# Kernel optimization log

Measured on AMD Instinct MI355X. Metric: run time of the kernel, lower is better.

## Reference

```python
import jax, jax.numpy as jnp
import numpy as np

NUM_QUANTS = 256
RES_CH = 120
SKIP_CH = 240
K = 2
NUM_BLOCKS = 16
CYCLE = 8
DILATIONS = [2 ** (i % CYCLE) for i in range(NUM_BLOCKS)]


def causal_conv1d(x, w, b, dilation=1):
    # x: [B, Cin, T], w: [Cout, Cin, K], left-pad for causality
    pad = (w.shape[-1] - 1) * dilation
    y = jax.lax.conv_general_dilated(
        x, w, window_strides=(1,), padding=[(pad, 0)],
        rhs_dilation=(dilation,), dimension_numbers=('NCH', 'OIH', 'NCH'))
    return y + b[None, :, None]


def setup_inputs() -> dict:
    key = jax.random.key(0)
    ks = jax.random.split(key, 16)
    B, T = 8, 16384
    s = 0.1
    inp = {
        'waveforms': jax.random.normal(ks[0], (B, T), jnp.float32),
        'W_in': jax.random.normal(ks[1], (RES_CH, 1, 1), jnp.float32) * s,
        'b_in': jnp.zeros((RES_CH,), jnp.float32),
        'Wf': jax.random.normal(ks[2], (NUM_BLOCKS, RES_CH, RES_CH, K), jnp.float32) * s,
        'bf': jnp.zeros((NUM_BLOCKS, RES_CH), jnp.float32),
        'Wg': jax.random.normal(ks[3], (NUM_BLOCKS, RES_CH, RES_CH, K), jnp.float32) * s,
        'bg': jnp.zeros((NUM_BLOCKS, RES_CH), jnp.float32),
        'Wres': jax.random.normal(ks[4], (NUM_BLOCKS, RES_CH, RES_CH, 1), jnp.float32) * s,
        'bres': jnp.zeros((NUM_BLOCKS, RES_CH), jnp.float32),
        'Wskip': jax.random.normal(ks[5], (NUM_BLOCKS, SKIP_CH, RES_CH, 1), jnp.float32) * s,
        'bskip': jnp.zeros((NUM_BLOCKS, SKIP_CH), jnp.float32),
        'W1': jax.random.normal(ks[6], (NUM_QUANTS, SKIP_CH, 1), jnp.float32) * s,
        'b1': jnp.zeros((NUM_QUANTS,), jnp.float32),
        'W2': jax.random.normal(ks[7], (NUM_QUANTS, NUM_QUANTS, 1), jnp.float32) * s,
        'b2': jnp.zeros((NUM_QUANTS,), jnp.float32),
    }
    return inp


def reference(waveforms, W_in, b_in, Wf, bf, Wg, bg, Wres, bres, Wskip, bskip, W1, b1, W2, b2):
    # input 1x1 conv: [B, T] -> [B, RES_CH, T]
    x = causal_conv1d(waveforms[:, None, :], W_in, b_in)
    skip_sum = jnp.zeros((x.shape[0], SKIP_CH, x.shape[2]), x.dtype)
    for i in range(NUM_BLOCKS):
        d = DILATIONS[i]
        f = jnp.tanh(causal_conv1d(x, Wf[i], bf[i], d))
        g = jax.nn.sigmoid(causal_conv1d(x, Wg[i], bg[i], d))
        z = f * g  # gated activation
        skip_sum = skip_sum + causal_conv1d(z, Wskip[i], bskip[i])
        x = x + causal_conv1d(z, Wres[i], bres[i])
    h = jax.nn.relu(skip_sum)
    h = jax.nn.relu(causal_conv1d(h, W1, b1))
    logits = causal_conv1d(h, W2, b2)  # [B, NUM_QUANTS, T]
    return logits
```

## Files before the change

kernel.cpp:

```cpp
#include <hip/hip_runtime.h>
#include <cstddef>

#define TT 16384
#define NBATCH 8
#define CH 128
#define RES 120
#define SKIPC 240
#define NQ 256
#define NT 64
#define KZ 2048

typedef __attribute__((ext_vector_type(8))) short bf8;
typedef __attribute__((ext_vector_type(4))) short s4;
typedef __attribute__((ext_vector_type(4))) float f32x4;

__device__ __forceinline__ short f2bf(float f) {
  unsigned u = __builtin_bit_cast(unsigned, f);
  u += 0x7fffu + ((u >> 16) & 1u);
  return (short)(u >> 16);
}
__device__ __forceinline__ float bf2f(short s) {
  unsigned u = ((unsigned)(unsigned short)s) << 16;
  return __builtin_bit_cast(float, u);
}

__global__ void k_pack(const float* __restrict__ Wf, const float* __restrict__ Wg,
                       const float* __restrict__ Wres, const float* __restrict__ Wskip,
                       const float* __restrict__ W1, const float* __restrict__ W2,
                       const float* __restrict__ bf, const float* __restrict__ bg,
                       const float* __restrict__ bres, const float* __restrict__ bskip,
                       short* __restrict__ Afg, short* __restrict__ Ars,
                       short* __restrict__ W1p, short* __restrict__ W2p,
                       float* __restrict__ biasp,
                       short* __restrict__ Wskp, float* __restrict__ bsum, int do2) {
  const int NAFG = 16 * 256 * 256;
  const int NARS = 16 * 384 * 128;
  const int NW = 256 * 256;
  const int NBIA = 16 * (128 * 3 + 256);
  const int NWSK = 256 * 2048;
  const int total = NAFG + NARS + 2 * NW + NBIA + NWSK + 256;
  for (int idx = blockIdx.x * blockDim.x + threadIdx.x; idx < total;
       idx += gridDim.x * blockDim.x) {
    if (idx < NAFG) {
      int i = idx >> 16, rem = idx & 65535, m = rem >> 8, k = rem & 255;
      int tap = k >> 7, ci = k & 127;
      float v = 0.f;
      if (ci < 120) {
        if (m < 120) v = Wf[((i * 120 + m) * 120 + ci) * 2 + tap];
        else if (m >= 128 && m < 248) v = Wg[((i * 120 + (m - 128)) * 120 + ci) * 2 + tap];
      }
      Afg[idx] = f2bf(v);
    } else if (idx < NAFG + NARS) {
      int j = idx - NAFG;
      int i = j / 49152, rem = j % 49152, m = rem >> 7, k = rem & 127;
      float v = 0.f;
      if (k < 120) {
        if (m < 120) v = Wres[(i * 120 + m) * 120 + k];
        else if (m >= 128 && m < 368) v = Wskip[(i * 240 + (m - 128)) * 120 + k];
      }
      Ars[j] = f2bf(v);
    } else if (idx < NAFG + NARS + NW) {
      int j = idx - NAFG - NARS, q = j >> 8, k = j & 255;
      W1p[j] = f2bf(k < 240 ? W1[q * 240 + k] : 0.f);
    } else if (idx < NAFG + NARS + 2 * NW) {
      int j = idx - NAFG - NARS - NW;
      W2p[j] = f2bf(W2[j]);
    } else if (idx < NAFG + NARS + 2 * NW + NBIA) {
      int j = idx - NAFG - NARS - 2 * NW;
      float v = 0.f;
      if (j < 2048) { int i = j >> 7, c = j & 127; if (c < 120) v = bf[i * 120 + c]; }
      else if (j < 4096) { int jj = j - 2048; int i = jj >> 7, c = jj & 127; if (c < 120) v = bg[i * 120 + c]; }
      else if (j < 6144) { int jj = j - 4096; int i = jj >> 7, c = jj & 127; if (c < 120) v = bres[i * 120 + c]; }
      else { int jj = j - 6144; int i = jj >> 8, c = jj & 255; if (c < 240) v = bskip[i * 240 + c]; }
      biasp[j] = v;
    } else if (idx < NAFG + NARS + 2 * NW + NBIA + NWSK) {
      if (do2) {
        int j = idx - NAFG - NARS - 2 * NW - NBIA;
        int m = j >> 11, k = j & 2047;
        int layer = k >> 7, ci = k & 127;
        float v = 0.f;
        if (m < 240 && ci < 120) v = Wskip[((size_t)layer * 240 + m) * 120 + ci];
        Wskp[j] = f2bf(v);
      }
    } else {
      if (do2) {
        int m = idx - (NAFG + NARS + 2 * NW + NBIA + NWSK);
        float v = 0.f;
        if (m < 240)
          for (int l = 0; l < 16; l++) v += bskip[l * 240 + m];
        bsum[m] = v;
      }
    }
  }
}

__global__ void k_input(const float* __restrict__ wave, const float* __restrict__ win,
                        const float* __restrict__ bin, short* __restrict__ x0) {
  int idx = blockIdx.x * blockDim.x + threadIdx.x;
  if (idx >= NBATCH * TT) return;
  float wv = wave[idx];
  short* row = x0 + (size_t)idx * CH;
  for (int c = 0; c < CH; c += 4) {
    s4 v;
#pragma unroll
    for (int j = 0; j < 4; j++)
      v[j] = (c + j < 120) ? f2bf(win[c + j] * wv + bin[c + j]) : (short)0;
    *(s4*)(row + c) = v;
  }
}

__global__ __launch_bounds__(256) void k_res2(
    const short* __restrict__ xin, short* __restrict__ xout,
    short* __restrict__ zg,
    const short* __restrict__ Afg, const short* __restrict__ Ars,
    const float* __restrict__ biasp, int layer, int dil, int b_off) {
  __shared__ short zT[NT][136];
  const int bl = blockIdx.y;
  const int b = b_off + bl;
  const int t0 = blockIdx.x * NT;
  const int tid = threadIdx.x;
  const int lane = tid & 63, w = tid >> 6;
  const int l15 = lane & 15, l4 = lane >> 4;
  const size_t xbase = (size_t)b * TT * CH;

  f32x4 fa[2][4], ga[2][4];
#pragma unroll
  for (int i = 0; i < 2; i++)
#pragma unroll
    for (int j = 0; j < 4; j++) { fa[i][j] = (f32x4)0.f; ga[i][j] = (f32x4)0.f; }

  const short* pBd[4];
  const short* pBc[4];
  bool vld[4];
#pragma unroll
  for (int nt = 0; nt < 4; nt++) {
    int t = t0 + nt * 16 + l15;
    int ts = t - dil;
    vld[nt] = (ts >= 0);
    pBd[nt] = xin + xbase + (size_t)(vld[nt] ? ts : 0) * CH + l4 * 8;
    pBc[nt] = xin + xbase + (size_t)t * CH + l4 * 8;
  }
  const short* pAf[2];
  const short* pAg[2];
#pragma unroll
  for (int mt = 0; mt < 2; mt++) {
    pAf[mt] = Afg + (size_t)(w * 32 + mt * 16 + l15) * 256 + l4 * 8;
    pAg[mt] = Afg + (size_t)(128 + w * 32 + mt * 16 + l15) * 256 + l4 * 8;
  }
  const bf8 zv = (bf8)(short)0;
#pragma unroll
  for (int kk = 0; kk < 8; kk++) {
    const int k = kk * 32;
    bf8 Bv[4];
#pragma unroll
    for (int nt = 0; nt < 4; nt++) {
      if (kk < 4) {
        bf8 v = *(const bf8*)(pBd[nt] + k);
        Bv[nt] = vld[nt] ? v : zv;
      } else {
        Bv[nt] = *(const bf8*)(pBc[nt] + (k - 128));
      }
    }
#pragma unroll
    for (int mt = 0; mt < 2; mt++) {
      bf8 Av = *(const bf8*)(pAf[mt] + k);
      bf8 Gv = *(const bf8*)(pAg[mt] + k);
#pragma unroll
      for (int nt = 0; nt < 4; nt++) {
        fa[mt][nt] = __builtin_amdgcn_mfma_f32_16x16x32_bf16(Av, Bv[nt], fa[mt][nt], 0, 0, 0);
        ga[mt][nt] = __builtin_amdgcn_mfma_f32_16x16x32_bf16(Gv, Bv[nt], ga[mt][nt], 0, 0, 0);
      }
    }
  }

  const float* bf_ = biasp + (size_t)layer * 128;
  const float* bg_ = biasp + 2048 + (size_t)layer * 128;
#pragma unroll
  for (int mt = 0; mt < 2; mt++) {
    int mb = w * 32 + mt * 16 + l4 * 4;
#pragma unroll
    for (int nt = 0; nt < 4; nt++) {
      s4 zp;
#pragma unroll
      for (int r = 0; r < 4; r++) {
        float f = fa[mt][nt][r] + bf_[mb + r];
        float g = ga[mt][nt][r] + bg_[mb + r];
        float th = 1.f - 2.f / (__expf(2.f * f) + 1.f);
        float sg = 1.f / (1.f + __expf(-g));
        zp[r] = f2bf(th * sg);
      }
      *(s4*)&zT[nt * 16 + l15][mb] = zp;
    }
  }
  __syncthreads();

  for (int u = tid; u < NT * 16; u += 256) {
    int t = u >> 4, c8 = u & 15;
    bf8 v = *(const bf8*)&zT[t][c8 * 8];
    *(bf8*)(zg + ((size_t)(bl * TT + t0 + t) * 16 + layer) * 128 + c8 * 8) = v;
  }

  f32x4 acc[2][4];
#pragma unroll
  for (int i = 0; i < 2; i++)
#pragma unroll
    for (int j = 0; j < 4; j++) acc[i][j] = (f32x4)0.f;
  const short* pA[2];
#pragma unroll
  for (int mt = 0; mt < 2; mt++)
    pA[mt] = Ars + (size_t)(w * 32 + mt * 16 + l15) * 128 + l4 * 8;
#pragma unroll
  for (int kk = 0; kk < 4; kk++) {
    const int k = kk * 32;
    bf8 Bv[4];
#pragma unroll
    for (int nt = 0; nt < 4; nt++) Bv[nt] = *(const bf8*)&zT[nt * 16 + l15][k + l4 * 8];
#pragma unroll
    for (int mt = 0; mt < 2; mt++) {
      bf8 Av = *(const bf8*)(pA[mt] + k);
#pragma unroll
      for (int nt = 0; nt < 4; nt++)
        acc[mt][nt] = __builtin_amdgcn_mfma_f32_16x16x32_bf16(Av, Bv[nt], acc[mt][nt], 0, 0, 0);
    }
  }

  const float* br_ = biasp + 4096 + (size_t)layer * 128;
#pragma unroll
  for (int mt = 0; mt < 2; mt++) {
    int m = w * 32 + mt * 16 + l4 * 4;
#pragma unroll
    for (int nt = 0; nt < 4; nt++) {
      int t = t0 + nt * 16 + l15;
      s4 xv = *(const s4*)(xin + xbase + (size_t)t * CH + m);
      s4 ov;
#pragma unroll
      for (int r = 0; r < 4; r++)
        ov[r] = f2bf(bf2f(xv[r]) + acc[mt][nt][r] + br_[m + r]);
      *(s4*)(xout + xbase + (size_t)t * CH + m) = ov;
    }
  }
}

__global__ __launch_bounds__(256) void k_head2(
    const short* __restrict__ zg, const short* __restrict__ Wskp,
    const float* __restrict__ bsum,
    const short* __restrict__ W1p, const float* __restrict__ b1,
    const short* __restrict__ W2p, const float* __restrict__ b2,
    float* __restrict__ out, int b_off) {
  __shared__ short hT[NT][264];
  const int bl = blockIdx.y;
  const int b = b_off + bl;
  const int t0 = blockIdx.x * NT;
  const int tid = threadIdx.x;
  const int lane = tid & 63, w = tid >> 6;
  const int l15 = lane & 15, l4 = lane >> 4;

  f32x4 acc[4][4];
#pragma unroll
  for (int i = 0; i < 4; i++)
#pragma unroll
    for (int j = 0; j < 4; j++) acc[i][j] = (f32x4)0.f;

  const short* pB[4];
#pragma unroll
  for (int nt = 0; nt < 4; nt++)
    pB[nt] = zg + (size_t)(bl * TT + t0 + nt * 16 + l15) * KZ + l4 * 8;
  const short* pA[4];
#pragma unroll
  for (int mt = 0; mt < 4; mt++)
    pA[mt] = Wskp + (size_t)(w * 64 + mt * 16 + l15) * KZ + l4 * 8;
  for (int kk = 0; kk < KZ / 32; kk++) {
    const int k = kk * 32;
    bf8 Bv[4];
#pragma unroll
    for (int nt = 0; nt < 4; nt++) Bv[nt] = *(const bf8*)(pB[nt] + k);
#pragma unroll
    for (int mt = 0; mt < 4; mt++) {
      bf8 Av = *(const bf8*)(pA[mt] + k);
#pragma unroll
      for (int nt = 0; nt < 4; nt++)
        acc[mt][nt] = __builtin_amdgcn_mfma_f32_16x16x32_bf16(Av, Bv[nt], acc[mt][nt], 0, 0, 0);
    }
  }
#pragma unroll
  for (int mt = 0; mt < 4; mt++) {
    int mb = w * 64 + mt * 16 + l4 * 4;
#pragma unroll
    for (int nt = 0; nt < 4; nt++) {
      s4 hp;
#pragma unroll
      for (int r = 0; r < 4; r++)
        hp[r] = f2bf(fmaxf(acc[mt][nt][r] + bsum[mb + r], 0.f));
      *(s4*)&hT[nt * 16 + l15][mb] = hp;
    }
  }
  __syncthreads();

#pragma unroll
  for (int i = 0; i < 4; i++)
#pragma unroll
    for (int j = 0; j < 4; j++) acc[i][j] = (f32x4)0.f;
#pragma unroll
  for (int kk = 0; kk < 8; kk++) {
    const int k = kk * 32;
    bf8 Bv[4];
#pragma unroll
    for (int nt = 0; nt < 4; nt++) Bv[nt] = *(const bf8*)&hT[nt * 16 + l15][k + l4 * 8];
#pragma unroll
    for (int mt = 0; mt < 4; mt++) {
      bf8 Av = *(const bf8*)(W1p + (size_t)(w * 64 + mt * 16 + l15) * 256 + k + l4 * 8);
#pragma unroll
      for (int nt = 0; nt < 4; nt++)
        acc[mt][nt] = __builtin_amdgcn_mfma_f32_16x16x32_bf16(Av, Bv[nt], acc[mt][nt], 0, 0, 0);
    }
  }
  __syncthreads();
#pragma unroll
  for (int mt = 0; mt < 4; mt++) {
    int mb = w * 64 + mt * 16 + l4 * 4;
#pragma unroll
    for (int nt = 0; nt < 4; nt++) {
      s4 hp;
#pragma unroll
      for (int r = 0; r < 4; r++)
        hp[r] = f2bf(fmaxf(acc[mt][nt][r] + b1[mb + r], 0.f));
      *(s4*)&hT[nt * 16 + l15][mb] = hp;
    }
  }
  __syncthreads();

#pragma unroll
  for (int i = 0; i < 4; i++)
#pragma unroll
    for (int j = 0; j < 4; j++) acc[i][j] = (f32x4)0.f;
#pragma unroll
  for (int kk = 0; kk < 8; kk++) {
    const int k = kk * 32;
    bf8 Bv[4];
#pragma unroll
    for (int nt = 0; nt < 4; nt++) Bv[nt] = *(const bf8*)&hT[nt * 16 + l15][k + l4 * 8];
#pragma unroll
    for (int mt = 0; mt < 4; mt++) {
      bf8 Av = *(const bf8*)(W2p + (size_t)(w * 64 + mt * 16 + l15) * 256 + k + l4 * 8);
#pragma unroll
      for (int nt = 0; nt < 4; nt++)
        acc[mt][nt] = __builtin_amdgcn_mfma_f32_16x16x32_bf16(Av, Bv[nt], acc[mt][nt], 0, 0, 0);
    }
  }
#pragma unroll
  for (int mt = 0; mt < 4; mt++) {
    int q = w * 64 + mt * 16 + l4 * 4;
#pragma unroll
    for (int nt = 0; nt < 4; nt++) {
      int t = t0 + nt * 16 + l15;
#pragma unroll
      for (int r = 0; r < 4; r++)
        out[((size_t)b * NQ + q + r) * TT + t] = acc[mt][nt][r] + b2[q + r];
    }
  }
}

__global__ __launch_bounds__(256) void k_res_mfma(
    const short* __restrict__ xin, short* __restrict__ xout,
    float* __restrict__ skip,
    const short* __restrict__ Afg, const short* __restrict__ Ars,
    const float* __restrict__ biasp, int layer, int dil, int first) {
  __shared__ short zT[NT][136];
  const int b = blockIdx.y;
  const int t0 = blockIdx.x * NT;
  const int tid = threadIdx.x;
  const int lane = tid & 63, w = tid >> 6;
  const int l15 = lane & 15, l4 = lane >> 4;
  const size_t xbase = (size_t)b * TT * CH;

  f32x4 fa[2][4], ga[2][4];
#pragma unroll
  for (int i = 0; i < 2; i++)
#pragma unroll
    for (int j = 0; j < 4; j++) { fa[i][j] = (f32x4)0.f; ga[i][j] = (f32x4)0.f; }

  const short* pBd[4];
  const short* pBc[4];
  bool vld[4];
#pragma unroll
  for (int nt = 0; nt < 4; nt++) {
    int t = t0 + nt * 16 + l15;
    int ts = t - dil;
    vld[nt] = (ts >= 0);
    pBd[nt] = xin + xbase + (size_t)(vld[nt] ? ts : 0) * CH + l4 * 8;
    pBc[nt] = xin + xbase + (size_t)t * CH + l4 * 8;
  }
  const short* pAf[2];
  const short* pAg[2];
#pragma unroll
  for (int mt = 0; mt < 2; mt++) {
    pAf[mt] = Afg + (size_t)(w * 32 + mt * 16 + l15) * 256 + l4 * 8;
    pAg[mt] = Afg + (size_t)(128 + w * 32 + mt * 16 + l15) * 256 + l4 * 8;
  }
  const bf8 zv = (bf8)(short)0;
#pragma unroll
  for (int kk = 0; kk < 8; kk++) {
    const int k = kk * 32;
    bf8 Bv[4];
#pragma unroll
    for (int nt = 0; nt < 4; nt++) {
      if (kk < 4) {
        bf8 v = *(const bf8*)(pBd[nt] + k);
        Bv[nt] = vld[nt] ? v : zv;
      } else {
        Bv[nt] = *(const bf8*)(pBc[nt] + (k - 128));
      }
    }
#pragma unroll
    for (int mt = 0; mt < 2; mt++) {
      bf8 Av = *(const bf8*)(pAf[mt] + k);
      bf8 Gv = *(const bf8*)(pAg[mt] + k);
#pragma unroll
      for (int nt = 0; nt < 4; nt++) {
        fa[mt][nt] = __builtin_amdgcn_mfma_f32_16x16x32_bf16(Av, Bv[nt], fa[mt][nt], 0, 0, 0);
        ga[mt][nt] = __builtin_amdgcn_mfma_f32_16x16x32_bf16(Gv, Bv[nt], ga[mt][nt], 0, 0, 0);
      }
    }
  }

  const float* bf_ = biasp + (size_t)layer * 128;
  const float* bg_ = biasp + 2048 + (size_t)layer * 128;
#pragma unroll
  for (int mt = 0; mt < 2; mt++) {
    int mb = w * 32 + mt * 16 + l4 * 4;
#pragma unroll
    for (int nt = 0; nt < 4; nt++) {
      s4 zp;
#pragma unroll
      for (int r = 0; r < 4; r++) {
        float f = fa[mt][nt][r] + bf_[mb + r];
        float g = ga[mt][nt][r] + bg_[mb + r];
        float th = 1.f - 2.f / (__expf(2.f * f) + 1.f);
        float sg = 1.f / (1.f + __expf(-g));
        zp[r] = f2bf(th * sg);
      }
      *(s4*)&zT[nt * 16 + l15][mb] = zp;
    }
  }
  __syncthreads();

  f32x4 acc[6][4];
#pragma unroll
  for (int i = 0; i < 6; i++)
#pragma unroll
    for (int j = 0; j < 4; j++) acc[i][j] = (f32x4)0.f;
  const short* pA[6];
#pragma unroll
  for (int mt = 0; mt < 6; mt++)
    pA[mt] = Ars + (size_t)(w * 96 + mt * 16 + l15) * 128 + l4 * 8;
#pragma unroll
  for (int kk = 0; kk < 4; kk++) {
    const int k = kk * 32;
    bf8 Bv[4];
#pragma unroll
    for (int nt = 0; nt < 4; nt++) Bv[nt] = *(const bf8*)&zT[nt * 16 + l15][k + l4 * 8];
#pragma unroll
    for (int mt = 0; mt < 6; mt++) {
      bf8 Av = *(const bf8*)(pA[mt] + k);
#pragma unroll
      for (int nt = 0; nt < 4; nt++)
        acc[mt][nt] = __builtin_amdgcn_mfma_f32_16x16x32_bf16(Av, Bv[nt], acc[mt][nt], 0, 0, 0);
    }
  }

  const float* br_ = biasp + 4096 + (size_t)layer * 128;
  const float* bs_ = biasp + 6144 + (size_t)layer * 256;
#pragma unroll
  for (int mt = 0; mt < 6; mt++) {
    int m = w * 96 + mt * 16 + l4 * 4;
#pragma unroll
    for (int nt = 0; nt < 4; nt++) {
      int t = t0 + nt * 16 + l15;
      if (m < 128) {
        s4 xv = *(const s4*)(xin + xbase + (size_t)t * CH + m);
        s4 ov;
#pragma unroll
        for (int r = 0; r < 4; r++)
          ov[r] = f2bf(bf2f(xv[r]) + acc[mt][nt][r] + br_[m + r]);
        *(s4*)(xout + xbase + (size_t)t * CH + m) = ov;
      } else if (m < 128 + SKIPC) {
        int c = m - 128;
        float* sp = skip + ((size_t)b * NQ + c) * TT + t;
#pragma unroll
        for (int r = 0; r < 4; r++) {
          float v = acc[mt][nt][r] + bs_[c + r];
          if (!first) v += sp[(size_t)r * TT];
          sp[(size_t)r * TT] = v;
        }
      }
    }
  }
}

__global__ __launch_bounds__(256) void k_head_mfma(
    const float* skip, const short* __restrict__ W1p, const float* __restrict__ b1,
    const short* __restrict__ W2p, const float* __restrict__ b2, float* out) {
  __shared__ short hT[NT][264];
  __shared__ short h2T[NT][264];
  const int b = blockIdx.y;
  const int t0 = blockIdx.x * NT;
  const int tid = threadIdx.x;
  const int lane = tid & 63, w = tid >> 6;
  const int l15 = lane & 15, l4 = lane >> 4;

  for (int u = tid; u < 256 * 16; u += 256) {
    int c = u >> 4, tq = u & 15;
    if (c < SKIPC) {
      f32x4 v = *(const f32x4*)(skip + ((size_t)b * NQ + c) * TT + t0 + tq * 4);
#pragma unroll
      for (int j = 0; j < 4; j++) hT[tq * 4 + j][c] = f2bf(fmaxf(v[j], 0.f));
    } else {
#pragma unroll
      for (int j = 0; j < 4; j++) hT[tq * 4 + j][c] = 0;
    }
  }
  __syncthreads();

  f32x4 acc[4][4];
#pragma unroll
  for (int i = 0; i < 4; i++)
#pragma unroll
    for (int j = 0; j < 4; j++) acc[i][j] = (f32x4)0.f;
#pragma unroll
  for (int kk = 0; kk < 8; kk++) {
    const int k = kk * 32;
    bf8 Bv[4];
#pragma unroll
    for (int nt = 0; nt < 4; nt++) Bv[nt] = *(const bf8*)&hT[nt * 16 + l15][k + l4 * 8];
#pragma unroll
    for (int mt = 0; mt < 4; mt++) {
      bf8 Av = *(const bf8*)(W1p + (size_t)(w * 64 + mt * 16 + l15) * 256 + k + l4 * 8);
#pragma unroll
      for (int nt = 0; nt < 4; nt++)
        acc[mt][nt] = __builtin_amdgcn_mfma_f32_16x16x32_bf16(Av, Bv[nt], acc[mt][nt], 0, 0, 0);
    }
  }
#pragma unroll
  for (int mt = 0; mt < 4; mt++) {
    int mb = w * 64 + mt * 16 + l4 * 4;
#pragma unroll
    for (int nt = 0; nt < 4; nt++) {
      s4 hp;
#pragma unroll
      for (int r = 0; r < 4; r++) hp[r] = f2bf(fmaxf(acc[mt][nt][r] + b1[mb + r], 0.f));
      *(s4*)&h2T[nt * 16 + l15][mb] = hp;
    }
  }
  __syncthreads();

#pragma unroll
  for (int i = 0; i < 4; i++)
#pragma unroll
    for (int j = 0; j < 4; j++) acc[i][j] = (f32x4)0.f;
#pragma unroll
  for (int kk = 0; kk < 8; kk++) {
    const int k = kk * 32;
    bf8 Bv[4];
#pragma unroll
    for (int nt = 0; nt < 4; nt++) Bv[nt] = *(const bf8*)&h2T[nt * 16 + l15][k + l4 * 8];
#pragma unroll
    for (int mt = 0; mt < 4; mt++) {
      bf8 Av = *(const bf8*)(W2p + (size_t)(w * 64 + mt * 16 + l15) * 256 + k + l4 * 8);
#pragma unroll
      for (int nt = 0; nt < 4; nt++)
        acc[mt][nt] = __builtin_amdgcn_mfma_f32_16x16x32_bf16(Av, Bv[nt], acc[mt][nt], 0, 0, 0);
    }
  }
#pragma unroll
  for (int mt = 0; mt < 4; mt++) {
    int q = w * 64 + mt * 16 + l4 * 4;
#pragma unroll
    for (int nt = 0; nt < 4; nt++) {
      int t = t0 + nt * 16 + l15;
#pragma unroll
      for (int r = 0; r < 4; r++)
        out[((size_t)b * NQ + q + r) * TT + t] = acc[mt][nt][r] + b2[q + r];
    }
  }
}

extern "C" void kernel_launch(void* const* d_in, const int* in_sizes, int n_in,
                              void* d_out, int out_size, void* d_ws, size_t ws_size,
                              hipStream_t stream) {
  const float* wave  = (const float*)d_in[0];
  const float* W_in  = (const float*)d_in[1];
  const float* b_in  = (const float*)d_in[2];
  const float* Wf    = (const float*)d_in[3];
  const float* bf    = (const float*)d_in[4];
  const float* Wg    = (const float*)d_in[5];
  const float* bg    = (const float*)d_in[6];
  const float* Wres  = (const float*)d_in[7];
  const float* bres  = (const float*)d_in[8];
  const float* Wskip = (const float*)d_in[9];
  const float* bskip = (const float*)d_in[10];
  const float* W1    = (const float*)d_in[11];
  const float* b1    = (const float*)d_in[12];
  const float* W2    = (const float*)d_in[13];
  const float* b2    = (const float*)d_in[14];
  float* out = (float*)d_out;

  char* ws = (char*)d_ws;
  short* xA    = (short*)ws;
  short* xB    = (short*)(ws + 33554432);
  short* Afg   = (short*)(ws + 67108864);
  short* Ars   = (short*)(ws + 69206016);
  short* W1p   = (short*)(ws + 70778880);
  short* W2p   = (short*)(ws + 70909952);
  float* biasp = (float*)(ws + 71041024);
  short* Wskp  = (short*)(ws + 71081984);
  float* bsum  = (float*)(ws + 72130560);
  short* zg    = (short*)(ws + 72131584);
  const size_t BASE = 72131584ull;
  const size_t ZPB  = (size_t)TT * KZ * 2;

  int nbg = 0;
  if      (ws_size >= BASE + 8 * ZPB) nbg = 8;
  else if (ws_size >= BASE + 4 * ZPB) nbg = 4;
  else if (ws_size >= BASE + 2 * ZPB) nbg = 2;
  else if (ws_size >= BASE + 1 * ZPB) nbg = 1;
  const int do2 = (ws_size >= BASE) ? 1 : 0;

  k_pack<<<1024, 256, 0, stream>>>(Wf, Wg, Wres, Wskip, W1, W2, bf, bg, bres, bskip,
                                   Afg, Ars, W1p, W2p, biasp, Wskp, bsum, do2);
  k_input<<<(NBATCH * TT) / 256, 256, 0, stream>>>(wave, W_in, b_in, xA);

  static const int dils[16] = {1, 2, 4, 8, 16, 32, 64, 128,
                               1, 2, 4, 8, 16, 32, 64, 128};
  if (nbg > 0) {
    for (int g = 0; g < NBATCH; g += nbg) {
      const short* xi = xA;
      short* xo = xB;
      for (int i = 0; i < 16; i++) {
        k_res2<<<dim3(TT / NT, nbg), 256, 0, stream>>>(
            xi, xo, zg, Afg + (size_t)i * 65536, Ars + (size_t)i * 49152,
            biasp, i, dils[i], g);
        short* tmp = (short*)xi; xi = xo; xo = tmp;
      }
      k_head2<<<dim3(TT / NT, nbg), 256, 0, stream>>>(zg, Wskp, bsum, W1p, b1,
                                                      W2p, b2, out, g);
    }
  } else {
    const short* xi = xA;
    short* xo = xB;
    for (int i = 0; i < 16; i++) {
      k_res_mfma<<<dim3(TT / NT, NBATCH), 256, 0, stream>>>(
          xi, xo, out, Afg + (size_t)i * 65536, Ars + (size_t)i * 49152,
          biasp, i, dils[i], i == 0 ? 1 : 0);
      short* tmp = (short*)xi; xi = xo; xo = tmp;
    }
    k_head_mfma<<<dim3(TT / NT, NBATCH), 256, 0, stream>>>(out, W1p, b1, W2p, b2, out);
  }
}
```

Before: 2.278 ms.

## Halve time tiles, stage inputs in LDS, double-buffer skip GEMM in head

Reduces the time tile of the residual and head kernels from 64 to 32 so twice as many blocks launch. The residual kernel now stages the current and dilated input rows in shared memory and reuses the staged current row for the residual add, instead of reloading from global memory. The head kernel double-buffers 256-wide chunks of the gated activations in shared memory rather than reading them directly from global. The zg and output stores become nontemporal. Smaller tiles reload weights more often per output, and the extra LDS use may lower occupancy.

```diff
diff --git a/kernel.cpp b/kernel.cpp
--- a/kernel.cpp
+++ b/kernel.cpp
@@ -7,7 +7,8 @@
 #define RES 120
 #define SKIPC 240
 #define NQ 256
-#define NT 64
+#define NT2 32
+#define NTF 64
 #define KZ 2048
 
 typedef __attribute__((ext_vector_type(8))) short bf8;
@@ -114,10 +115,280 @@
     short* __restrict__ zg,
     const short* __restrict__ Afg, const short* __restrict__ Ars,
     const float* __restrict__ biasp, int layer, int dil, int b_off) {
-  __shared__ short zT[NT][136];
+  __shared__ short xc[NT2][136];
+  __shared__ short xd[NT2][136];
+  __shared__ short zT[NT2][136];
   const int bl = blockIdx.y;
   const int b = b_off + bl;
-  const int t0 = blockIdx.x * NT;
+  const int t0 = blockIdx.x * NT2;
+  const int tid = threadIdx.x;
+  const int lane = tid & 63, w = tid >> 6;
+  const int l15 = lane & 15, l4 = lane >> 4;
+  const size_t xbase = (size_t)b * TT * CH;
+
+#pragma unroll
+  for (int j = 0; j < 2; j++) {
+    int i = tid + j * 256;
+    int t = i >> 4, c8 = i & 15;
+    *(bf8*)&xc[t][c8 * 8] = *(const bf8*)(xin + xbase + (size_t)(t0 + t) * CH + c8 * 8);
+    int ts = t0 + t - dil;
+    bf8 vd = (bf8)(short)0;
+    if (ts >= 0) vd = *(const bf8*)(xin + xbase + (size_t)ts * CH + c8 * 8);
+    *(bf8*)&xd[t][c8 * 8] = vd;
+  }
+  __syncthreads();
+
+  f32x4 fa[2][2], ga[2][2];
+#pragma unroll
+  for (int i = 0; i < 2; i++)
+#pragma unroll
+    for (int j = 0; j < 2; j++) { fa[i][j] = (f32x4)0.f; ga[i][j] = (f32x4)0.f; }
+  const short* pAf[2];
+  const short* pAg[2];
+#pragma unroll
+  for (int mt = 0; mt < 2; mt++) {
+    pAf[mt] = Afg + (size_t)(w * 32 + mt * 16 + l15) * 256 + l4 * 8;
+    pAg[mt] = Afg + (size_t)(128 + w * 32 + mt * 16 + l15) * 256 + l4 * 8;
+  }
+#pragma unroll
+  for (int kk = 0; kk < 8; kk++) {
+    const int k = kk * 32;
+    bf8 Bv[2];
+#pragma unroll
+    for (int nt = 0; nt < 2; nt++)
+      Bv[nt] = (kk < 4) ? *(const bf8*)&xd[nt * 16 + l15][k + l4 * 8]
+                        : *(const bf8*)&xc[nt * 16 + l15][(k - 128) + l4 * 8];
+#pragma unroll
+    for (int mt = 0; mt < 2; mt++) {
+      bf8 Av = *(const bf8*)(pAf[mt] + k);
+      bf8 Gv = *(const bf8*)(pAg[mt] + k);
+#pragma unroll
+      for (int nt = 0; nt < 2; nt++) {
+        fa[mt][nt] = __builtin_amdgcn_mfma_f32_16x16x32_bf16(Av, Bv[nt], fa[mt][nt], 0, 0, 0);
+        ga[mt][nt] = __builtin_amdgcn_mfma_f32_16x16x32_bf16(Gv, Bv[nt], ga[mt][nt], 0, 0, 0);
+      }
+    }
+  }
+
+  const float* bf_ = biasp + (size_t)layer * 128;
+  const float* bg_ = biasp + 2048 + (size_t)layer * 128;
+#pragma unroll
+  for (int mt = 0; mt < 2; mt++) {
+    const int mb = w * 32 + mt * 16 + l4 * 4;
+#pragma unroll
+    for (int nt = 0; nt < 2; nt++) {
+      s4 zp;
+#pragma unroll
+      for (int r = 0; r < 4; r++) {
+        float f = fa[mt][nt][r] + bf_[mb + r];
+        float g = ga[mt][nt][r] + bg_[mb + r];
+        float th = 1.f - 2.f / (__expf(2.f * f) + 1.f);
+        float sg = 1.f / (1.f + __expf(-g));
+        zp[r] = f2bf(th * sg);
+      }
+      *(s4*)&zT[nt * 16 + l15][mb] = zp;
+    }
+  }
+  __syncthreads();
+
+#pragma unroll
+  for (int j = 0; j < 2; j++) {
+    int i = tid + j * 256;
+    int t = i >> 4, c8 = i & 15;
+    bf8 v = *(const bf8*)&zT[t][c8 * 8];
+    __builtin_nontemporal_store(
+        v, (bf8*)(zg + ((size_t)(bl * TT + t0 + t) * 16 + layer) * 128 + c8 * 8));
+  }
+
+  f32x4 acc[2][2];
+#pragma unroll
+  for (int i = 0; i < 2; i++)
+#pragma unroll
+    for (int j = 0; j < 2; j++) acc[i][j] = (f32x4)0.f;
+  const short* pA[2];
+#pragma unroll
+  for (int mt = 0; mt < 2; mt++)
+    pA[mt] = Ars + (size_t)(w * 32 + mt * 16 + l15) * 128 + l4 * 8;
+#pragma unroll
+  for (int kk = 0; kk < 4; kk++) {
+    const int k = kk * 32;
+    bf8 Bv[2];
+#pragma unroll
+    for (int nt = 0; nt < 2; nt++) Bv[nt] = *(const bf8*)&zT[nt * 16 + l15][k + l4 * 8];
+#pragma unroll
+    for (int mt = 0; mt < 2; mt++) {
+      bf8 Av = *(const bf8*)(pA[mt] + k);
+#pragma unroll
+      for (int nt = 0; nt < 2; nt++)
+        acc[mt][nt] = __builtin_amdgcn_mfma_f32_16x16x32_bf16(Av, Bv[nt], acc[mt][nt], 0, 0, 0);
+    }
+  }
+
+  const float* br_ = biasp + 4096 + (size_t)layer * 128;
+#pragma unroll
+  for (int mt = 0; mt < 2; mt++) {
+    const int m = w * 32 + mt * 16 + l4 * 4;
+#pragma unroll
+    for (int nt = 0; nt < 2; nt++) {
+      int t = t0 + nt * 16 + l15;
+      s4 xv = *(const s4*)&xc[nt * 16 + l15][m];
+      s4 ov;
+#pragma unroll
+      for (int r = 0; r < 4; r++)
+        ov[r] = f2bf(bf2f(xv[r]) + acc[mt][nt][r] + br_[m + r]);
+      *(s4*)(xout + xbase + (size_t)t * CH + m) = ov;
+    }
+  }
+}
+
+__global__ __launch_bounds__(256) void k_head2(
+    const short* __restrict__ zg, const short* __restrict__ Wskp,
+    const float* __restrict__ bsum,
+    const short* __restrict__ W1p, const float* __restrict__ b1,
+    const short* __restrict__ W2p, const float* __restrict__ b2,
+    float* __restrict__ out, int b_off) {
+  __shared__ short bufA[NT2][264];
+  __shared__ short bufB[NT2][264];
+  const int bl = blockIdx.y;
+  const int b = b_off + bl;
+  const int t0 = blockIdx.x * NT2;
+  const int tid = threadIdx.x;
+  const int lane = tid & 63, w = tid >> 6;
+  const int l15 = lane & 15, l4 = lane >> 4;
+
+  f32x4 acc[4][2];
+#pragma unroll
+  for (int i = 0; i < 4; i++)
+#pragma unroll
+    for (int j = 0; j < 2; j++) acc[i][j] = (f32x4)0.f;
+
+  const short* zrow = zg + (size_t)(bl * TT + t0) * KZ;
+
+#pragma unroll
+  for (int j = 0; j < 4; j++) {
+    int i = tid + j * 256;
+    int t = i >> 5, c8 = i & 31;
+    *(bf8*)&bufA[t][c8 * 8] = *(const bf8*)(zrow + (size_t)t * KZ + c8 * 8);
+  }
+  __syncthreads();
+  for (int c = 0; c < 8; c++) {
+    short (*cur)[264] = (c & 1) ? bufB : bufA;
+    short (*nxt)[264] = (c & 1) ? bufA : bufB;
+    if (c < 7) {
+#pragma unroll
+      for (int j = 0; j < 4; j++) {
+        int i = tid + j * 256;
+        int t = i >> 5, c8 = i & 31;
+        *(bf8*)&nxt[t][c8 * 8] =
+            *(const bf8*)(zrow + (size_t)t * KZ + (c + 1) * 256 + c8 * 8);
+      }
+    }
+#pragma unroll
+    for (int kk = 0; kk < 8; kk++) {
+      const int k = kk * 32;
+      bf8 Bv[2];
+#pragma unroll
+      for (int nt = 0; nt < 2; nt++)
+        Bv[nt] = *(const bf8*)&cur[nt * 16 + l15][k + l4 * 8];
+#pragma unroll
+      for (int mt = 0; mt < 4; mt++) {
+        bf8 Av = *(const bf8*)(Wskp + (size_t)(w * 64 + mt * 16 + l15) * KZ +
+                               c * 256 + k + l4 * 8);
+#pragma unroll
+        for (int nt = 0; nt < 2; nt++)
+          acc[mt][nt] = __builtin_amdgcn_mfma_f32_16x16x32_bf16(Av, Bv[nt], acc[mt][nt], 0, 0, 0);
+      }
+    }
+    __syncthreads();
+  }
+
+#pragma unroll
+  for (int mt = 0; mt < 4; mt++) {
+    const int mb = w * 64 + mt * 16 + l4 * 4;
+#pragma unroll
+    for (int nt = 0; nt < 2; nt++) {
+      s4 hp;
+#pragma unroll
+      for (int r = 0; r < 4; r++)
+        hp[r] = f2bf(fmaxf(acc[mt][nt][r] + bsum[mb + r], 0.f));
+      *(s4*)&bufA[nt * 16 + l15][mb] = hp;
+    }
+  }
+  __syncthreads();
+
+#pragma unroll
+  for (int i = 0; i < 4; i++)
+#pragma unroll
+    for (int j = 0; j < 2; j++) acc[i][j] = (f32x4)0.f;
+#pragma unroll
+  for (int kk = 0; kk < 8; kk++) {
+    const int k = kk * 32;
+    bf8 Bv[2];
+#pragma unroll
+    for (int nt = 0; nt < 2; nt++) Bv[nt] = *(const bf8*)&bufA[nt * 16 + l15][k + l4 * 8];
+#pragma unroll
+    for (int mt = 0; mt < 4; mt++) {
+      bf8 Av = *(const bf8*)(W1p + (size_t)(w * 64 + mt * 16 + l15) * 256 + k + l4 * 8);
+#pragma unroll
+      for (int nt = 0; nt < 2; nt++)
+        acc[mt][nt] = __builtin_amdgcn_mfma_f32_16x16x32_bf16(Av, Bv[nt], acc[mt][nt], 0, 0, 0);
+    }
+  }
+#pragma unroll
+  for (int mt = 0; mt < 4; mt++) {
+    const int mb = w * 64 + mt * 16 + l4 * 4;
+#pragma unroll
+    for (int nt = 0; nt < 2; nt++) {
+      s4 hp;
+#pragma unroll
+      for (int r = 0; r < 4; r++)
+        hp[r] = f2bf(fmaxf(acc[mt][nt][r] + b1[mb + r], 0.f));
+      *(s4*)&bufB[nt * 16 + l15][mb] = hp;
+    }
+  }
+  __syncthreads();
+
+#pragma unroll
+  for (int i = 0; i < 4; i++)
+#pragma unroll
+    for (int j = 0; j < 2; j++) acc[i][j] = (f32x4)0.f;
+#pragma unroll
+  for (int kk = 0; kk < 8; kk++) {
+    const int k = kk * 32;
+    bf8 Bv[2];
+#pragma unroll
+    for (int nt = 0; nt < 2; nt++) Bv[nt] = *(const bf8*)&bufB[nt * 16 + l15][k + l4 * 8];
+#pragma unroll
+    for (int mt = 0; mt < 4; mt++) {
+      bf8 Av = *(const bf8*)(W2p + (size_t)(w * 64 + mt * 16 + l15) * 256 + k + l4 * 8);
+#pragma unroll
+      for (int nt = 0; nt < 2; nt++)
+        acc[mt][nt] = __builtin_amdgcn_mfma_f32_16x16x32_bf16(Av, Bv[nt], acc[mt][nt], 0, 0, 0);
+    }
+  }
+#pragma unroll
+  for (int mt = 0; mt < 4; mt++) {
+    const int q = w * 64 + mt * 16 + l4 * 4;
+#pragma unroll
+    for (int nt = 0; nt < 2; nt++) {
+      int t = t0 + nt * 16 + l15;
+#pragma unroll
+      for (int r = 0; r < 4; r++) {
+        float v = acc[mt][nt][r] + b2[q + r];
+        __builtin_nontemporal_store(v, out + ((size_t)b * NQ + q + r) * TT + t);
+      }
+    }
+  }
+}
+
+__global__ __launch_bounds__(256) void k_res_mfma(
+    const short* __restrict__ xin, short* __restrict__ xout,
+    float* __restrict__ skip,
+    const short* __restrict__ Afg, const short* __restrict__ Ars,
+    const float* __restrict__ biasp, int layer, int dil, int first) {
+  __shared__ short zT[NTF][136];
+  const int b = blockIdx.y;
+  const int t0 = blockIdx.x * NTF;
   const int tid = threadIdx.x;
   const int lane = tid & 63, w = tid >> 6;
   const int l15 = lane & 15, l4 = lane >> 4;
@@ -194,256 +465,6 @@
   }
   __syncthreads();
 
-  for (int u = tid; u < NT * 16; u += 256) {
-    int t = u >> 4, c8 = u & 15;
-    bf8 v = *(const bf8*)&zT[t][c8 * 8];
-    *(bf8*)(zg + ((size_t)(bl * TT + t0 + t) * 16 + layer) * 128 + c8 * 8) = v;
-  }
-
-  f32x4 acc[2][4];
-#pragma unroll
-  for (int i = 0; i < 2; i++)
-#pragma unroll
-    for (int j = 0; j < 4; j++) acc[i][j] = (f32x4)0.f;
-  const short* pA[2];
-#pragma unroll
-  for (int mt = 0; mt < 2; mt++)
-    pA[mt] = Ars + (size_t)(w * 32 + mt * 16 + l15) * 128 + l4 * 8;
-#pragma unroll
-  for (int kk = 0; kk < 4; kk++) {
-    const int k = kk * 32;
-    bf8 Bv[4];
-#pragma unroll
-    for (int nt = 0; nt < 4; nt++) Bv[nt] = *(const bf8*)&zT[nt * 16 + l15][k + l4 * 8];
-#pragma unroll
-    for (int mt = 0; mt < 2; mt++) {
-      bf8 Av = *(const bf8*)(pA[mt] + k);
-#pragma unroll
-      for (int nt = 0; nt < 4; nt++)
-        acc[mt][nt] = __builtin_amdgcn_mfma_f32_16x16x32_bf16(Av, Bv[nt], acc[mt][nt], 0, 0, 0);
-    }
-  }
-
-  const float* br_ = biasp + 4096 + (size_t)layer * 128;
-#pragma unroll
-  for (int mt = 0; mt < 2; mt++) {
-    int m = w * 32 + mt * 16 + l4 * 4;
-#pragma unroll
-    for (int nt = 0; nt < 4; nt++) {
-      int t = t0 + nt * 16 + l15;
-      s4 xv = *(const s4*)(xin + xbase + (size_t)t * CH + m);
-      s4 ov;
-#pragma unroll
-      for (int r = 0; r < 4; r++)
-        ov[r] = f2bf(bf2f(xv[r]) + acc[mt][nt][r] + br_[m + r]);
-      *(s4*)(xout + xbase + (size_t)t * CH + m) = ov;
-    }
-  }
-}
-
-__global__ __launch_bounds__(256) void k_head2(
-    const short* __restrict__ zg, const short* __restrict__ Wskp,
-    const float* __restrict__ bsum,
-    const short* __restrict__ W1p, const float* __restrict__ b1,
-    const short* __restrict__ W2p, const float* __restrict__ b2,
-    float* __restrict__ out, int b_off) {
-  __shared__ short hT[NT][264];
-  const int bl = blockIdx.y;
-  const int b = b_off + bl;
-  const int t0 = blockIdx.x * NT;
-  const int tid = threadIdx.x;
-  const int lane = tid & 63, w = tid >> 6;
-  const int l15 = lane & 15, l4 = lane >> 4;
-
-  f32x4 acc[4][4];
-#pragma unroll
-  for (int i = 0; i < 4; i++)
-#pragma unroll
-    for (int j = 0; j < 4; j++) acc[i][j] = (f32x4)0.f;
-
-  const short* pB[4];
-#pragma unroll
-  for (int nt = 0; nt < 4; nt++)
-    pB[nt] = zg + (size_t)(bl * TT + t0 + nt * 16 + l15) * KZ + l4 * 8;
-  const short* pA[4];
-#pragma unroll
-  for (int mt = 0; mt < 4; mt++)
-    pA[mt] = Wskp + (size_t)(w * 64 + mt * 16 + l15) * KZ + l4 * 8;
-  for (int kk = 0; kk < KZ / 32; kk++) {
-    const int k = kk * 32;
-    bf8 Bv[4];
-#pragma unroll
-    for (int nt = 0; nt < 4; nt++) Bv[nt] = *(const bf8*)(pB[nt] + k);
-#pragma unroll
-    for (int mt = 0; mt < 4; mt++) {
-      bf8 Av = *(const bf8*)(pA[mt] + k);
-#pragma unroll
-      for (int nt = 0; nt < 4; nt++)
-        acc[mt][nt] = __builtin_amdgcn_mfma_f32_16x16x32_bf16(Av, Bv[nt], acc[mt][nt], 0, 0, 0);
-    }
-  }
-#pragma unroll
-  for (int mt = 0; mt < 4; mt++) {
-    int mb = w * 64 + mt * 16 + l4 * 4;
-#pragma unroll
-    for (int nt = 0; nt < 4; nt++) {
-      s4 hp;
-#pragma unroll
-      for (int r = 0; r < 4; r++)
-        hp[r] = f2bf(fmaxf(acc[mt][nt][r] + bsum[mb + r], 0.f));
-      *(s4*)&hT[nt * 16 + l15][mb] = hp;
-    }
-  }
-  __syncthreads();
-
-#pragma unroll
-  for (int i = 0; i < 4; i++)
-#pragma unroll
-    for (int j = 0; j < 4; j++) acc[i][j] = (f32x4)0.f;
-#pragma unroll
-  for (int kk = 0; kk < 8; kk++) {
-    const int k = kk * 32;
-    bf8 Bv[4];
-#pragma unroll
-    for (int nt = 0; nt < 4; nt++) Bv[nt] = *(const bf8*)&hT[nt * 16 + l15][k + l4 * 8];
-#pragma unroll
-    for (int mt = 0; mt < 4; mt++) {
-      bf8 Av = *(const bf8*)(W1p + (size_t)(w * 64 + mt * 16 + l15) * 256 + k + l4 * 8);
-#pragma unroll
-      for (int nt = 0; nt < 4; nt++)
-        acc[mt][nt] = __builtin_amdgcn_mfma_f32_16x16x32_bf16(Av, Bv[nt], acc[mt][nt], 0, 0, 0);
-    }
-  }
-  __syncthreads();
-#pragma unroll
-  for (int mt = 0; mt < 4; mt++) {
-    int mb = w * 64 + mt * 16 + l4 * 4;
-#pragma unroll
-    for (int nt = 0; nt < 4; nt++) {
-      s4 hp;
-#pragma unroll
-      for (int r = 0; r < 4; r++)
-        hp[r] = f2bf(fmaxf(acc[mt][nt][r] + b1[mb + r], 0.f));
-      *(s4*)&hT[nt * 16 + l15][mb] = hp;
-    }
-  }
-  __syncthreads();
-
-#pragma unroll
-  for (int i = 0; i < 4; i++)
-#pragma unroll
-    for (int j = 0; j < 4; j++) acc[i][j] = (f32x4)0.f;
-#pragma unroll
-  for (int kk = 0; kk < 8; kk++) {
-    const int k = kk * 32;
-    bf8 Bv[4];
-#pragma unroll
-    for (int nt = 0; nt < 4; nt++) Bv[nt] = *(const bf8*)&hT[nt * 16 + l15][k + l4 * 8];
-#pragma unroll
-    for (int mt = 0; mt < 4; mt++) {
-      bf8 Av = *(const bf8*)(W2p + (size_t)(w * 64 + mt * 16 + l15) * 256 + k + l4 * 8);
-#pragma unroll
-      for (int nt = 0; nt < 4; nt++)
-        acc[mt][nt] = __builtin_amdgcn_mfma_f32_16x16x32_bf16(Av, Bv[nt], acc[mt][nt], 0, 0, 0);
-    }
-  }
-#pragma unroll
-  for (int mt = 0; mt < 4; mt++) {
-    int q = w * 64 + mt * 16 + l4 * 4;
-#pragma unroll
-    for (int nt = 0; nt < 4; nt++) {
-      int t = t0 + nt * 16 + l15;
-#pragma unroll
-      for (int r = 0; r < 4; r++)
-        out[((size_t)b * NQ + q + r) * TT + t] = acc[mt][nt][r] + b2[q + r];
-    }
-  }
-}
-
-__global__ __launch_bounds__(256) void k_res_mfma(
-    const short* __restrict__ xin, short* __restrict__ xout,
-    float* __restrict__ skip,
-    const short* __restrict__ Afg, const short* __restrict__ Ars,
-    const float* __restrict__ biasp, int layer, int dil, int first) {
-  __shared__ short zT[NT][136];
-  const int b = blockIdx.y;
-  const int t0 = blockIdx.x * NT;
-  const int tid = threadIdx.x;
-  const int lane = tid & 63, w = tid >> 6;
-  const int l15 = lane & 15, l4 = lane >> 4;
-  const size_t xbase = (size_t)b * TT * CH;
-
-  f32x4 fa[2][4], ga[2][4];
-#pragma unroll
-  for (int i = 0; i < 2; i++)
-#pragma unroll
-    for (int j = 0; j < 4; j++) { fa[i][j] = (f32x4)0.f; ga[i][j] = (f32x4)0.f; }
-
-  const short* pBd[4];
-  const short* pBc[4];
-  bool vld[4];
-#pragma unroll
-  for (int nt = 0; nt < 4; nt++) {
-    int t = t0 + nt * 16 + l15;
-    int ts = t - dil;
-    vld[nt] = (ts >= 0);
-    pBd[nt] = xin + xbase + (size_t)(vld[nt] ? ts : 0) * CH + l4 * 8;
-    pBc[nt] = xin + xbase + (size_t)t * CH + l4 * 8;
-  }
-  const short* pAf[2];
-  const short* pAg[2];
-#pragma unroll
-  for (int mt = 0; mt < 2; mt++) {
-    pAf[mt] = Afg + (size_t)(w * 32 + mt * 16 + l15) * 256 + l4 * 8;
-    pAg[mt] = Afg + (size_t)(128 + w * 32 + mt * 16 + l15) * 256 + l4 * 8;
-  }
-  const bf8 zv = (bf8)(short)0;
-#pragma unroll
-  for (int kk = 0; kk < 8; kk++) {
-    const int k = kk * 32;
-    bf8 Bv[4];
-#pragma unroll
-    for (int nt = 0; nt < 4; nt++) {
-      if (kk < 4) {
-        bf8 v = *(const bf8*)(pBd[nt] + k);
-        Bv[nt] = vld[nt] ? v : zv;
-      } else {
-        Bv[nt] = *(const bf8*)(pBc[nt] + (k - 128));
-      }
-    }
-#pragma unroll
-    for (int mt = 0; mt < 2; mt++) {
-      bf8 Av = *(const bf8*)(pAf[mt] + k);
-      bf8 Gv = *(const bf8*)(pAg[mt] + k);
-#pragma unroll
-      for (int nt = 0; nt < 4; nt++) {
-        fa[mt][nt] = __builtin_amdgcn_mfma_f32_16x16x32_bf16(Av, Bv[nt], fa[mt][nt], 0, 0, 0);
-        ga[mt][nt] = __builtin_amdgcn_mfma_f32_16x16x32_bf16(Gv, Bv[nt], ga[mt][nt], 0, 0, 0);
-      }
-    }
-  }
-
-  const float* bf_ = biasp + (size_t)layer * 128;
-  const float* bg_ = biasp + 2048 + (size_t)layer * 128;
-#pragma unroll
-  for (int mt = 0; mt < 2; mt++) {
-    int mb = w * 32 + mt * 16 + l4 * 4;
-#pragma unroll
-    for (int nt = 0; nt < 4; nt++) {
-      s4 zp;
-#pragma unroll
-      for (int r = 0; r < 4; r++) {
-        float f = fa[mt][nt][r] + bf_[mb + r];
-        float g = ga[mt][nt][r] + bg_[mb + r];
-        float th = 1.f - 2.f / (__expf(2.f * f) + 1.f);
-        float sg = 1.f / (1.f + __expf(-g));
-        zp[r] = f2bf(th * sg);
-      }
-      *(s4*)&zT[nt * 16 + l15][mb] = zp;
-    }
-  }
-  __syncthreads();
-
   f32x4 acc[6][4];
 #pragma unroll
   for (int i = 0; i < 6; i++)
@@ -500,10 +521,10 @@
 __global__ __launch_bounds__(256) void k_head_mfma(
     const float* skip, const short* __restrict__ W1p, const float* __restrict__ b1,
     const short* __restrict__ W2p, const float* __restrict__ b2, float* out) {
-  __shared__ short hT[NT][264];
-  __shared__ short h2T[NT][264];
+  __shared__ short hT[NTF][264];
+  __shared__ short h2T[NTF][264];
   const int b = blockIdx.y;
-  const int t0 = blockIdx.x * NT;
+  const int t0 = blockIdx.x * NTF;
   const int tid = threadIdx.x;
   const int lane = tid & 63, w = tid >> 6;
   const int l15 = lane & 15, l4 = lane >> 4;
@@ -623,10 +644,10 @@
   else if (ws_size >= BASE + 4 * ZPB) nbg = 4;
   else if (ws_size >= BASE + 2 * ZPB) nbg = 2;
   else if (ws_size >= BASE + 1 * ZPB) nbg = 1;
-  const int do2 = (ws_size >= BASE) ? 1 : 0;
 
   k_pack<<<1024, 256, 0, stream>>>(Wf, Wg, Wres, Wskip, W1, W2, bf, bg, bres, bskip,
-                                   Afg, Ars, W1p, W2p, biasp, Wskp, bsum, do2);
+                                   Afg, Ars, W1p, W2p, biasp, Wskp, bsum,
+                                   nbg > 0 ? 1 : 0);
   k_input<<<(NBATCH * TT) / 256, 256, 0, stream>>>(wave, W_in, b_in, xA);
 
   static const int dils[16] = {1, 2, 4, 8, 16, 32, 64, 128,
@@ -636,23 +657,23 @@
       const short* xi = xA;
       short* xo = xB;
       for (int i = 0; i < 16; i++) {
-        k_res2<<<dim3(TT / NT, nbg), 256, 0, stream>>>(
+        k_res2<<<dim3(TT / NT2, nbg), 256, 0, stream>>>(
             xi, xo, zg, Afg + (size_t)i * 65536, Ars + (size_t)i * 49152,
             biasp, i, dils[i], g);
         short* tmp = (short*)xi; xi = xo; xo = tmp;
       }
-      k_head2<<<dim3(TT / NT, nbg), 256, 0, stream>>>(zg, Wskp, bsum, W1p, b1,
-                                                      W2p, b2, out, g);
+      k_head2<<<dim3(TT / NT2, nbg), 256, 0, stream>>>(zg, Wskp, bsum, W1p, b1,
+                                                       W2p, b2, out, g);
     }
   } else {
     const short* xi = xA;
     short* xo = xB;
     for (int i = 0; i < 16; i++) {
-      k_res_mfma<<<dim3(TT / NT, NBATCH), 256, 0, stream>>>(
+      k_res_mfma<<<dim3(TT / NTF, NBATCH), 256, 0, stream>>>(
           xi, xo, out, Afg + (size_t)i * 65536, Ars + (size_t)i * 49152,
           biasp, i, dils[i], i == 0 ? 1 : 0);
       short* tmp = (short*)xi; xi = xo; xo = tmp;
     }
-    k_head_mfma<<<dim3(TT / NT, NBATCH), 256, 0, stream>>>(out, W1p, b1, W2p, b2, out);
-  }
-}
+    k_head_mfma<<<dim3(TT / NTF, NBATCH), 256, 0, stream>>>(out, W1p, b1, W2p, b2, out);
+  }
+}
```

Result: slower. 2.500 ms (+9.7%).
